# Optimization experiments

Measured on AMD Instinct MI355X. Metric: run time of the kernel, lower is better.

Reference implementation:

```python
import jax, jax.numpy as jnp
import numpy as np

N_NODES = 50000
N_EDGES = 800000
HID = 256
HEADS = 4
HEAD_C = HID // HEADS  # 64
IN_CH = 16
OUT_CH = 4
NEG_SLOPE = 0.2  # PyG GATConv default LeakyReLU slope
LN_EPS = 1e-5


def setup_inputs() -> dict:
    key = jax.random.key(0)
    ks = jax.random.split(key, 12)
    s = 0.05
    return {
        "x": jax.random.normal(ks[0], (N_NODES, IN_CH), dtype=jnp.float32),
        "edge_index": jax.random.randint(ks[1], (2, N_EDGES), 0, N_NODES, dtype=jnp.int64),
        "w_in": jax.random.normal(ks[2], (IN_CH, HID), dtype=jnp.float32) * s,
        "b_in": jnp.zeros((HID,), dtype=jnp.float32),
        "w_gat": jax.random.normal(ks[3], (4, HID, HID), dtype=jnp.float32) * s,
        "att_src": jax.random.normal(ks[4], (4, HEADS, HEAD_C), dtype=jnp.float32) * s,
        "att_dst": jax.random.normal(ks[5], (4, HEADS, HEAD_C), dtype=jnp.float32) * s,
        "b_gat": jnp.zeros((4, HID), dtype=jnp.float32),
        "ln_scale": jnp.ones((4, HID), dtype=jnp.float32),
        "ln_bias": jnp.zeros((4, HID), dtype=jnp.float32),
        "w_out": jax.random.normal(ks[6], (HID, OUT_CH), dtype=jnp.float32) * s,
        "b_out": jnp.zeros((OUT_CH,), dtype=jnp.float32),
    }


def _gat_layer(x, src, dst, W, a_src, a_dst, bias, g, beta):
    """One GATConv(concat, heads=4) + LayerNorm + ELU. x:[N,HID]."""
    n = x.shape[0]
    h = (x @ W).reshape(n, HEADS, HEAD_C)                 # [N,H,C]
    a_s = jnp.einsum("nhc,hc->nh", h, a_src)              # [N,H]
    a_d = jnp.einsum("nhc,hc->nh", h, a_dst)              # [N,H]
    logits = jax.nn.leaky_relu(a_s[src] + a_d[dst], NEG_SLOPE)  # [E,H]
    # segment softmax over destination neighborhoods (self-loops ensure non-empty)
    m = jax.ops.segment_max(logits, dst, num_segments=n)
    e = jnp.exp(logits - m[dst])
    denom = jax.ops.segment_sum(e, dst, num_segments=n)
    alpha = e / (denom[dst] + 1e-16)                      # [E,H]
    msg = alpha[:, :, None] * h[src]                      # [E,H,C]
    out = jax.ops.segment_sum(msg, dst, num_segments=n).reshape(n, HID) + bias
    mu = out.mean(-1, keepdims=True)
    var = out.var(-1, keepdims=True)
    out = (out - mu) * jax.lax.rsqrt(var + LN_EPS) * g + beta
    return jax.nn.elu(out)


def reference(x, edge_index, w_in, b_in, w_gat, att_src, att_dst, b_gat,
              ln_scale, ln_bias, w_out, b_out):
    n = x.shape[0]
    # PyG GATConv adds self-loops by default
    loops = jnp.arange(n, dtype=edge_index.dtype)
    ei = jnp.concatenate([edge_index, jnp.stack([loops, loops])], axis=1)
    src, dst = ei[0], ei[1]

    x = x @ w_in + b_in                                   # input_proj
    h = x
    for l in (0, 1):
        h = _gat_layer(h, src, dst, w_gat[l], att_src[l], att_dst[l],
                       b_gat[l], ln_scale[l], ln_bias[l])
    x = x + h
    h = x
    for l in (2, 3):
        h = _gat_layer(h, src, dst, w_gat[l], att_src[l], att_dst[l],
                       b_gat[l], ln_scale[l], ln_bias[l])
    x = x + h
    return x @ w_out + b_out
```

## Files before the change

kernel.cpp:

```cpp
#include <hip/hip_runtime.h>
#include <math.h>

#define NN 50000
#define E0 800000
#define ET 850000
#define HID 256
#define INCH 16
#define MAXDEG 64

#define NB_P1   416
#define EPB     2048
#define NBUCK   196

#define NB_WT   256
#define NB_IP   6250
#define NB_PREP (NB_P1 + NB_WT + NB_IP)

#define NB_G    782
#define NB_G0   (NBUCK + NB_G)

typedef _Float16 h8 __attribute__((ext_vector_type(8)));
typedef float f32x4 __attribute__((ext_vector_type(4)));

__device__ __forceinline__ void load_lds16(const void* g, void* l) {
    __builtin_amdgcn_global_load_lds(
        (const __attribute__((address_space(1))) unsigned int*)g,
        (__attribute__((address_space(3))) unsigned int*)l, 16, 0, 0);
}

__global__ __launch_bounds__(256) void prep_kernel(
    const float* __restrict__ w_gat, _Float16* __restrict__ WT,
    const float* __restrict__ x, const float* __restrict__ w_in,
    const float* __restrict__ b_in, _Float16* __restrict__ Ph,
    const int* __restrict__ ei, unsigned int* __restrict__ pairs,
    int* __restrict__ cnt_g, int* __restrict__ off_g) {
    __shared__ unsigned int hist[256], pref[256], cur2[256];
    int b = blockIdx.x, t = threadIdx.x;
    if (b < NB_P1) {
        hist[t] = 0;
        __syncthreads();
        unsigned int pk[8];
        int base = b * EPB + t;
#pragma unroll
        for (int k = 0; k < 8; ++k) {
            int e = base + k * 256;
            pk[k] = 0xFFFFFFFFu;
            if (e < ET) {
                int s, d;
                if (e < E0) { s = ei[e]; d = ei[E0 + e]; }
                else        { s = d = e - E0; }
                pk[k] = ((unsigned int)d << 16) | (unsigned int)s;
                atomicAdd(&hist[d >> 8], 1u);
            }
        }
        __syncthreads();
        unsigned int h = hist[t];
        pref[t] = h;
        __syncthreads();
#pragma unroll
        for (int o = 1; o < 256; o <<= 1) {
            unsigned int v = (t >= o) ? pref[t - o] : 0u;
            __syncthreads();
            pref[t] += v;
            __syncthreads();
        }
        unsigned int ex = pref[t] - h;
        cur2[t] = ex;
        if (t < NBUCK) {
            cnt_g[b * NBUCK + t] = (int)h;
            off_g[b * NBUCK + t] = (int)ex;
        }
        __syncthreads();
#pragma unroll
        for (int k = 0; k < 8; ++k) {
            if (pk[k] != 0xFFFFFFFFu) {
                unsigned int g = pk[k] >> 24;
                unsigned int pos = atomicAdd(&cur2[g], 1u);
                pairs[b * EPB + pos] = pk[k];
            }
        }
    } else if (b < NB_P1 + NB_WT) {
        int k = b - NB_P1;
#pragma unroll
        for (int l = 0; l < 4; ++l) {
            float v = w_gat[((size_t)l * 256 + k) * 256 + t];
            WT[((size_t)l * 256 + t) * 256 + k] = (_Float16)v;
        }
    } else {
        int ipb = b - NB_P1 - NB_WT;
        int sub = t >> 5, l32 = t & 31;
        int n = ipb * 8 + sub;
        int c0 = l32 * 8;
        const float* xr = x + n * INCH;
        float a[8];
#pragma unroll
        for (int k = 0; k < 8; k += 4) {
            float4 bb = *(const float4*)(b_in + c0 + k);
            a[k] = bb.x; a[k + 1] = bb.y; a[k + 2] = bb.z; a[k + 3] = bb.w;
        }
#pragma unroll
        for (int k = 0; k < INCH; ++k) {
            float xv = xr[k];
            const float4 w0 = *(const float4*)(w_in + k * 256 + c0);
            const float4 w1 = *(const float4*)(w_in + k * 256 + c0 + 4);
            a[0] += xv * w0.x; a[1] += xv * w0.y; a[2] += xv * w0.z; a[3] += xv * w0.w;
            a[4] += xv * w1.x; a[5] += xv * w1.y; a[6] += xv * w1.z; a[7] += xv * w1.w;
        }
        h8 o;
#pragma unroll
        for (int k = 0; k < 8; ++k) o[k] = (_Float16)a[k];
        *(h8*)(Ph + (size_t)n * 256 + c0) = o;
    }
}

__device__ __forceinline__ void gemm_tile(
    int rb, int cb,
    const _Float16* __restrict__ A, const _Float16* __restrict__ BT,
    _Float16* __restrict__ H, const float* __restrict__ att_s,
    const float* __restrict__ att_d, float* __restrict__ AS, float* __restrict__ AD,
    _Float16* As, _Float16* Bs) {
    int t = threadIdx.x;
    int wv = t >> 6, lane = t & 63;
    int wr = (wv >> 1) * 64, wc = (wv & 1) * 64;
    int lm = lane & 15, lq = lane >> 4;
    f32x4 acc[4][4] = {};

    int rch = lane >> 2;
    int q = lane & 3;

    for (int k0 = 0; k0 < 256; k0 += 32) {
#pragma unroll
        for (int c = 0; c < 2; ++c) {
            int r = wv * 32 + c * 16 + rch;
            int g = q ^ (r & 3);
            int ra = rb + r; if (ra >= NN) ra = NN - 1;
            load_lds16(A + (size_t)ra * 256 + k0 + g * 8,
                       (char*)As + wv * 2048 + c * 1024);
            load_lds16(BT + (size_t)(cb + r) * 256 + k0 + g * 8,
                       (char*)Bs + wv * 2048 + c * 1024);
        }
        __syncthreads();
        h8 af[4], bfr[4];
#pragma unroll
        for (int i = 0; i < 4; ++i) {
            int row = wr + i * 16 + lm;
            af[i] = *(const h8*)((const char*)As + row * 64 + ((lq ^ (row & 3)) * 16));
        }
#pragma unroll
        for (int j = 0; j < 4; ++j) {
            int row = wc + j * 16 + lm;
            bfr[j] = *(const h8*)((const char*)Bs + row * 64 + ((lq ^ (row & 3)) * 16));
        }
#pragma unroll
        for (int i = 0; i < 4; ++i)
#pragma unroll
            for (int j = 0; j < 4; ++j)
                acc[i][j] = __builtin_amdgcn_mfma_f32_16x16x32_f16(af[i], bfr[j], acc[i][j], 0, 0, 0);
        __syncthreads();
    }

    int head = (cb + wc) >> 6;
    float sa[4], sd[4];
#pragma unroll
    for (int j = 0; j < 4; ++j) {
        sa[j] = att_s[head * 64 + j * 16 + lm];
        sd[j] = att_d[head * 64 + j * 16 + lm];
    }
#pragma unroll
    for (int i = 0; i < 4; ++i)
#pragma unroll
        for (int rr = 0; rr < 4; ++rr) {
            float vs = acc[i][0][rr] * sa[0] + acc[i][1][rr] * sa[1]
                     + acc[i][2][rr] * sa[2] + acc[i][3][rr] * sa[3];
            float vd = acc[i][0][rr] * sd[0] + acc[i][1][rr] * sd[1]
                     + acc[i][2][rr] * sd[2] + acc[i][3][rr] * sd[3];
#pragma unroll
            for (int o = 1; o <= 8; o <<= 1) {
                vs += __shfl_xor(vs, o, 64);
                vd += __shfl_xor(vd, o, 64);
            }
            int row = rb + wr + i * 16 + lq * 4 + rr;
            if (lm == 0 && row < NN) {
                AS[row * 4 + head] = vs;
                AD[row * 4 + head] = vd;
            }
        }

#pragma unroll
    for (int i = 0; i < 4; ++i)
#pragma unroll
        for (int j = 0; j < 4; ++j) {
            int col = cb + wc + j * 16 + lm;
#pragma unroll
            for (int rr = 0; rr < 4; ++rr) {
                int row = rb + wr + i * 16 + lq * 4 + rr;
                if (row < NN) H[(size_t)row * 256 + col] = (_Float16)acc[i][j][rr];
            }
        }
}

__global__ __launch_bounds__(256) void gemm_fused_kernel(
    const _Float16* __restrict__ A, const _Float16* __restrict__ BT,
    _Float16* __restrict__ H, const float* __restrict__ att_s,
    const float* __restrict__ att_d, float* __restrict__ AS, float* __restrict__ AD) {
    __shared__ _Float16 As[128 * 32];
    __shared__ _Float16 Bs[128 * 32];
    gemm_tile(blockIdx.x * 128, blockIdx.y * 128, A, BT, H, att_s, att_d, AS, AD, As, Bs);
}

__global__ __launch_bounds__(256) void gemm0_p2_kernel(
    const _Float16* __restrict__ A, const _Float16* __restrict__ BT,
    _Float16* __restrict__ H, const float* __restrict__ att_s,
    const float* __restrict__ att_d, float* __restrict__ AS, float* __restrict__ AD,
    const unsigned int* __restrict__ pairs, const int* __restrict__ cnt_g,
    const int* __restrict__ off_g, int* __restrict__ cursor,
    unsigned short* __restrict__ csr_pad) {
    __shared__ _Float16 As[128 * 32];
    __shared__ _Float16 Bs[128 * 32];
    int b = blockIdx.x;
    if (b < NBUCK) {
        int g = b, t = threadIdx.x;
        unsigned int* curs = (unsigned int*)As;
        curs[t] = 0;
        __syncthreads();
        for (int sb = t; sb < NB_P1; sb += 256) {
            int c = cnt_g[sb * NBUCK + g];
            int o = off_g[sb * NBUCK + g];
            const unsigned int* p = pairs + sb * EPB + o;
            for (int i = 0; i < c; ++i) {
                unsigned int pk = p[i];
                int d = (int)(pk >> 16);
                unsigned int pos = atomicAdd(&curs[d & 255], 1u);
                if (pos < MAXDEG)
                    csr_pad[((size_t)d << 6) + pos] = (unsigned short)(pk & 0xFFFFu);
            }
        }
        __syncthreads();
        int n = (g << 8) + t;
        if (n < NN) cursor[n] = (int)curs[t];
        return;
    }
    int g2 = b - NBUCK;
    gemm_tile((g2 >> 1) * 128, (g2 & 1) * 128, A, BT, H, att_s, att_d, AS, AD, As, Bs);
}

__global__ __launch_bounds__(256) void agg_kernel(
    const _Float16* __restrict__ H, const float4* __restrict__ AS,
    const float4* __restrict__ AD,
    const int* __restrict__ cnt, const unsigned short* __restrict__ csr_pad,
    const float* __restrict__ bias, const float* __restrict__ g, const float* __restrict__ beta,
    const _Float16* __restrict__ res, _Float16* __restrict__ outh,
    const float* __restrict__ wout, const float* __restrict__ bout,
    float* __restrict__ out) {
    int t = threadIdx.x;
    int l32 = t & 31;
    int n = blockIdx.x * 8 + (t >> 5);
    int deg = cnt[n];
    if (deg > MAXDEG) deg = MAXDEG;
    int start = n << 6, end = start + deg;
    float4 adv = AD[n];
    int head = l32 >> 3;
    int c0 = l32 * 8;
    float advh = (head == 0) ? adv.x : (head == 1) ? adv.y : (head == 2) ? adv.z : adv.w;

    float acc[8] = {};
    float acc_e = 0.f;
#pragma unroll 4
    for (int i = start; i < end; ++i) {
        int s = csr_pad[i];
        const float* as = (const float*)&AS[s];
        float v = as[head] + advh;
        v = (v >= 0.f) ? v : 0.2f * v;
        float e = __expf(v);
        acc_e += e;
        h8 hv = *(const h8*)(H + (size_t)s * 256 + c0);
#pragma unroll
        for (int k = 0; k < 8; ++k) acc[k] += e * (float)hv[k];
    }
    float dinv = 1.f / (acc_e + 1e-16f);

    float val[8];
#pragma unroll
    for (int k = 0; k < 8; k += 4) {
        float4 bb = *(const float4*)(bias + c0 + k);
        val[k]     = acc[k]     * dinv + bb.x;
        val[k + 1] = acc[k + 1] * dinv + bb.y;
        val[k + 2] = acc[k + 2] * dinv + bb.z;
        val[k + 3] = acc[k + 3] * dinv + bb.w;
    }

    float s1 = 0.f, s2 = 0.f;
#pragma unroll
    for (int k = 0; k < 8; ++k) { s1 += val[k]; s2 += val[k] * val[k]; }
#pragma unroll
    for (int o = 16; o >= 1; o >>= 1) {
        s1 += __shfl_xor(s1, o, 64);
        s2 += __shfl_xor(s2, o, 64);
    }
    float mu = s1 * (1.f / 256.f);
    float var = s2 * (1.f / 256.f) - mu * mu;
    float rs = rsqrtf(var + 1e-5f);

    float y[8];
#pragma unroll
    for (int k = 0; k < 8; k += 4) {
        float4 g4 = *(const float4*)(g + c0 + k);
        float4 b4 = *(const float4*)(beta + c0 + k);
        y[k]     = (val[k]     - mu) * rs * g4.x + b4.x;
        y[k + 1] = (val[k + 1] - mu) * rs * g4.y + b4.y;
        y[k + 2] = (val[k + 2] - mu) * rs * g4.z + b4.z;
        y[k + 3] = (val[k + 3] - mu) * rs * g4.w + b4.w;
    }
#pragma unroll
    for (int k = 0; k < 8; ++k) y[k] = (y[k] > 0.f) ? y[k] : (__expf(y[k]) - 1.f);
    if (res) {
        h8 r0 = *(const h8*)(res + (size_t)n * 256 + c0);
#pragma unroll
        for (int k = 0; k < 8; ++k) y[k] += (float)r0[k];
    }
    if (wout) {
        float o0 = 0.f, o1 = 0.f, o2 = 0.f, o3 = 0.f;
#pragma unroll
        for (int k = 0; k < 8; ++k) {
            float4 wv = *(const float4*)(wout + (size_t)(c0 + k) * 4);
            o0 += y[k] * wv.x; o1 += y[k] * wv.y; o2 += y[k] * wv.z; o3 += y[k] * wv.w;
        }
#pragma unroll
        for (int o = 16; o >= 1; o >>= 1) {
            o0 += __shfl_xor(o0, o, 64);
            o1 += __shfl_xor(o1, o, 64);
            o2 += __shfl_xor(o2, o, 64);
            o3 += __shfl_xor(o3, o, 64);
        }
        if (l32 == 0) {
            float4 ov = make_float4(o0 + bout[0], o1 + bout[1], o2 + bout[2], o3 + bout[3]);
            *(float4*)(out + (size_t)n * 4) = ov;
        }
    } else {
        h8 o0;
#pragma unroll
        for (int k = 0; k < 8; ++k) o0[k] = (_Float16)y[k];
        *(h8*)(outh + (size_t)n * 256 + c0) = o0;
    }
}

extern "C" void kernel_launch(void* const* d_in, const int* in_sizes, int n_in,
                              void* d_out, int out_size, void* d_ws, size_t ws_size,
                              hipStream_t stream) {
    const float* x       = (const float*)d_in[0];
    const int*   ei      = (const int*)  d_in[1];
    const float* w_in    = (const float*)d_in[2];
    const float* b_in    = (const float*)d_in[3];
    const float* w_gat   = (const float*)d_in[4];
    const float* att_src = (const float*)d_in[5];
    const float* att_dst = (const float*)d_in[6];
    const float* b_gat   = (const float*)d_in[7];
    const float* ln_g    = (const float*)d_in[8];
    const float* ln_b    = (const float*)d_in[9];
    const float* w_out   = (const float*)d_in[10];
    const float* b_out   = (const float*)d_in[11];
    float* out = (float*)d_out;

    char* ws = (char*)d_ws;
    size_t off = 0;
    auto alloc = [&](size_t bytes) {
        void* p = ws + off;
        off += (bytes + 255) & ~(size_t)255;
        return p;
    };
    _Float16*       Ph      = (_Float16*)alloc((size_t)NN * HID * 2);
    _Float16*       Ch      = (_Float16*)alloc((size_t)NN * HID * 2);
    _Float16*       Gh      = (_Float16*)alloc((size_t)NN * HID * 2);
    _Float16*       H       = (_Float16*)alloc((size_t)NN * HID * 2);
    _Float16*       WT      = (_Float16*)alloc((size_t)4 * HID * HID * 2);
    float*          ASAD    = (float*)alloc((size_t)NN * 8 * 4);
    int*            cursor  = (int*)alloc((size_t)NN * 4);
    unsigned short* csr_pad = (unsigned short*)alloc((size_t)NN * MAXDEG * 2);
    unsigned int*   pairs   = (unsigned int*)alloc((size_t)NB_P1 * EPB * 4);
    int*            cnt_g   = (int*)alloc((size_t)NB_P1 * NBUCK * 4);
    int*            off_g   = (int*)alloc((size_t)NB_P1 * NBUCK * 4);

    float* AS = ASAD;
    float* AD = ASAD + (size_t)NN * 4;

    const dim3 GEMM_GRID(391, 2);
    const int NB_AGG = NN / 8;

    prep_kernel<<<NB_PREP, 256, 0, stream>>>(w_gat, WT, x, w_in, b_in, Ph,
                                             ei, pairs, cnt_g, off_g);

    gemm0_p2_kernel<<<NB_G0, 256, 0, stream>>>(
        Ph, WT, H, att_src, att_dst, AS, AD, pairs, cnt_g, off_g, cursor, csr_pad);
    agg_kernel<<<NB_AGG, 256, 0, stream>>>(
        H, (const float4*)AS, (const float4*)AD, cursor, csr_pad,
        b_gat, ln_g, ln_b, nullptr, Gh, nullptr, nullptr, nullptr);

    auto run_layer = [&](const _Float16* inh, int l, const _Float16* res, _Float16* outh,
                         const float* wo, const float* bo) {
        gemm_fused_kernel<<<GEMM_GRID, 256, 0, stream>>>(
            inh, WT + (size_t)l * HID * HID, H,
            att_src + l * 256, att_dst + l * 256, AS, AD);
        agg_kernel<<<NB_AGG, 256, 0, stream>>>(
            H, (const float4*)AS, (const float4*)AD, cursor, csr_pad,
            b_gat + l * 256, ln_g + l * 256, ln_b + l * 256, res, outh, wo, bo,
            wo ? out : nullptr);
    };

    run_layer(Gh, 1, Ph,      Ch, nullptr, nullptr);
    run_layer(Ch, 2, nullptr, Gh, nullptr, nullptr);
    run_layer(Gh, 3, Ch,      Ph, w_out,   b_out);
}
```

Baseline: 527.7 us.

## Assign one wavefront per node and precompute edge weights in LDS

The aggregation kernel now uses a full 64-lane wavefront per destination node instead of half a wave. Each lane loads 4 channels instead of 8. Before the gather loop, the lanes compute the neighbor indices and all four heads' exp(leaky_relu) logits in parallel and store them in LDS. This takes the per-edge AS load and exp off the serial gather loop and doubles the parallelism per node. In exchange it uses narrower 8-byte H loads, twice as many blocks, an extra reduction step, and some LDS usage. There is no barrier between the LDS writes and reads, which is safe only because each wave reads only its own region.

```diff
diff --git a/kernel.cpp b/kernel.cpp
--- a/kernel.cpp
+++ b/kernel.cpp
@@ -20,6 +20,7 @@
 #define NB_G0   (NBUCK + NB_G)
 
 typedef _Float16 h8 __attribute__((ext_vector_type(8)));
+typedef _Float16 h4 __attribute__((ext_vector_type(4)));
 typedef float f32x4 __attribute__((ext_vector_type(4)));
 
 __device__ __forceinline__ void load_lds16(const void* g, void* l) {
@@ -252,48 +253,58 @@
     const _Float16* __restrict__ res, _Float16* __restrict__ outh,
     const float* __restrict__ wout, const float* __restrict__ bout,
     float* __restrict__ out) {
+    __shared__ float eLs[4][256];
+    __shared__ int   sLs[4][64];
     int t = threadIdx.x;
-    int l32 = t & 31;
-    int n = blockIdx.x * 8 + (t >> 5);
+    int wv = t >> 6, lane = t & 63;
+    int n = blockIdx.x * 4 + wv;
+    int head = lane >> 4;
+    int c0 = lane * 4;
+    float* eL = eLs[wv];
+    int*   sL = sLs[wv];
+
     int deg = cnt[n];
     if (deg > MAXDEG) deg = MAXDEG;
-    int start = n << 6, end = start + deg;
     float4 adv = AD[n];
-    int head = l32 >> 3;
-    int c0 = l32 * 8;
-    float advh = (head == 0) ? adv.x : (head == 1) ? adv.y : (head == 2) ? adv.z : adv.w;
-
-    float acc[8] = {};
-    float acc_e = 0.f;
+
+    float4 e4 = make_float4(0.f, 0.f, 0.f, 0.f);
+    int sv = 0;
+    if (lane < deg) {
+        sv = csr_pad[(n << 6) + lane];
+        float4 as = AS[sv];
+        float v0 = as.x + adv.x; v0 = (v0 >= 0.f) ? v0 : 0.2f * v0;
+        float v1 = as.y + adv.y; v1 = (v1 >= 0.f) ? v1 : 0.2f * v1;
+        float v2 = as.z + adv.z; v2 = (v2 >= 0.f) ? v2 : 0.2f * v2;
+        float v3 = as.w + adv.w; v3 = (v3 >= 0.f) ? v3 : 0.2f * v3;
+        e4 = make_float4(__expf(v0), __expf(v1), __expf(v2), __expf(v3));
+    }
+    sL[lane] = sv;
+    *(float4*)(eL + c0) = e4;
+
+    float acc0 = 0.f, acc1 = 0.f, acc2 = 0.f, acc3 = 0.f, acc_e = 0.f;
 #pragma unroll 4
-    for (int i = start; i < end; ++i) {
-        int s = csr_pad[i];
-        const float* as = (const float*)&AS[s];
-        float v = as[head] + advh;
-        v = (v >= 0.f) ? v : 0.2f * v;
-        float e = __expf(v);
+    for (int i = 0; i < deg; ++i) {
+        float e = eL[i * 4 + head];
+        int s = sL[i];
+        h4 hv = *(const h4*)(H + (size_t)s * 256 + c0);
         acc_e += e;
-        h8 hv = *(const h8*)(H + (size_t)s * 256 + c0);
-#pragma unroll
-        for (int k = 0; k < 8; ++k) acc[k] += e * (float)hv[k];
+        acc0 += e * (float)hv[0];
+        acc1 += e * (float)hv[1];
+        acc2 += e * (float)hv[2];
+        acc3 += e * (float)hv[3];
     }
     float dinv = 1.f / (acc_e + 1e-16f);
 
-    float val[8];
-#pragma unroll
-    for (int k = 0; k < 8; k += 4) {
-        float4 bb = *(const float4*)(bias + c0 + k);
-        val[k]     = acc[k]     * dinv + bb.x;
-        val[k + 1] = acc[k + 1] * dinv + bb.y;
-        val[k + 2] = acc[k + 2] * dinv + bb.z;
-        val[k + 3] = acc[k + 3] * dinv + bb.w;
-    }
-
-    float s1 = 0.f, s2 = 0.f;
-#pragma unroll
-    for (int k = 0; k < 8; ++k) { s1 += val[k]; s2 += val[k] * val[k]; }
-#pragma unroll
-    for (int o = 16; o >= 1; o >>= 1) {
+    float4 bb = *(const float4*)(bias + c0);
+    float val0 = acc0 * dinv + bb.x;
+    float val1 = acc1 * dinv + bb.y;
+    float val2 = acc2 * dinv + bb.z;
+    float val3 = acc3 * dinv + bb.w;
+
+    float s1 = val0 + val1 + val2 + val3;
+    float s2 = val0 * val0 + val1 * val1 + val2 * val2 + val3 * val3;
+#pragma unroll
+    for (int o = 32; o >= 1; o >>= 1) {
         s1 += __shfl_xor(s1, o, 64);
         s2 += __shfl_xor(s2, o, 64);
     }
@@ -301,46 +312,45 @@
     float var = s2 * (1.f / 256.f) - mu * mu;
     float rs = rsqrtf(var + 1e-5f);
 
-    float y[8];
-#pragma unroll
-    for (int k = 0; k < 8; k += 4) {
-        float4 g4 = *(const float4*)(g + c0 + k);
-        float4 b4 = *(const float4*)(beta + c0 + k);
-        y[k]     = (val[k]     - mu) * rs * g4.x + b4.x;
-        y[k + 1] = (val[k + 1] - mu) * rs * g4.y + b4.y;
-        y[k + 2] = (val[k + 2] - mu) * rs * g4.z + b4.z;
-        y[k + 3] = (val[k + 3] - mu) * rs * g4.w + b4.w;
-    }
-#pragma unroll
-    for (int k = 0; k < 8; ++k) y[k] = (y[k] > 0.f) ? y[k] : (__expf(y[k]) - 1.f);
+    float4 g4 = *(const float4*)(g + c0);
+    float4 b4 = *(const float4*)(beta + c0);
+    float y0 = (val0 - mu) * rs * g4.x + b4.x;
+    float y1 = (val1 - mu) * rs * g4.y + b4.y;
+    float y2 = (val2 - mu) * rs * g4.z + b4.z;
+    float y3 = (val3 - mu) * rs * g4.w + b4.w;
+    y0 = (y0 > 0.f) ? y0 : (__expf(y0) - 1.f);
+    y1 = (y1 > 0.f) ? y1 : (__expf(y1) - 1.f);
+    y2 = (y2 > 0.f) ? y2 : (__expf(y2) - 1.f);
+    y3 = (y3 > 0.f) ? y3 : (__expf(y3) - 1.f);
     if (res) {
-        h8 r0 = *(const h8*)(res + (size_t)n * 256 + c0);
-#pragma unroll
-        for (int k = 0; k < 8; ++k) y[k] += (float)r0[k];
+        h4 r0 = *(const h4*)(res + (size_t)n * 256 + c0);
+        y0 += (float)r0[0]; y1 += (float)r0[1]; y2 += (float)r0[2]; y3 += (float)r0[3];
     }
     if (wout) {
-        float o0 = 0.f, o1 = 0.f, o2 = 0.f, o3 = 0.f;
-#pragma unroll
-        for (int k = 0; k < 8; ++k) {
-            float4 wv = *(const float4*)(wout + (size_t)(c0 + k) * 4);
-            o0 += y[k] * wv.x; o1 += y[k] * wv.y; o2 += y[k] * wv.z; o3 += y[k] * wv.w;
-        }
-#pragma unroll
-        for (int o = 16; o >= 1; o >>= 1) {
+        float4 w0 = *(const float4*)(wout + (size_t)(c0 + 0) * 4);
+        float4 w1 = *(const float4*)(wout + (size_t)(c0 + 1) * 4);
+        float4 w2 = *(const float4*)(wout + (size_t)(c0 + 2) * 4);
+        float4 w3 = *(const float4*)(wout + (size_t)(c0 + 3) * 4);
+        float o0 = y0 * w0.x + y1 * w1.x + y2 * w2.x + y3 * w3.x;
+        float o1 = y0 * w0.y + y1 * w1.y + y2 * w2.y + y3 * w3.y;
+        float o2 = y0 * w0.z + y1 * w1.z + y2 * w2.z + y3 * w3.z;
+        float o3 = y0 * w0.w + y1 * w1.w + y2 * w2.w + y3 * w3.w;
+#pragma unroll
+        for (int o = 32; o >= 1; o >>= 1) {
             o0 += __shfl_xor(o0, o, 64);
             o1 += __shfl_xor(o1, o, 64);
             o2 += __shfl_xor(o2, o, 64);
             o3 += __shfl_xor(o3, o, 64);
         }
-        if (l32 == 0) {
+        if (lane == 0) {
             float4 ov = make_float4(o0 + bout[0], o1 + bout[1], o2 + bout[2], o3 + bout[3]);
             *(float4*)(out + (size_t)n * 4) = ov;
         }
     } else {
-        h8 o0;
-#pragma unroll
-        for (int k = 0; k < 8; ++k) o0[k] = (_Float16)y[k];
-        *(h8*)(outh + (size_t)n * 256 + c0) = o0;
+        h4 o0;
+        o0[0] = (_Float16)y0; o0[1] = (_Float16)y1;
+        o0[2] = (_Float16)y2; o0[3] = (_Float16)y3;
+        *(h4*)(outh + (size_t)n * 256 + c0) = o0;
     }
 }
 
@@ -384,7 +394,7 @@
     float* AD = ASAD + (size_t)NN * 4;
 
     const dim3 GEMM_GRID(391, 2);
-    const int NB_AGG = NN / 8;
+    const int NB_AGG = NN / 4;
 
     prep_kernel<<<NB_PREP, 256, 0, stream>>>(w_gat, WT, x, w_in, b_in, Ph,
                                              ei, pairs, cnt_g, off_g);
```

Result: faster. 511.1 us (-3.1%).

## Double-buffer GEMM LDS, remap tiles, and precompute edge weights per wave in aggregation

Applied to the files above, without the earlier changes.

The GEMM tile loop now double-buffers its LDS staging, issuing the next K-slice's global-to-LDS loads before the current slice's MFMAs so load latency can overlap compute. Both GEMM kernels switch to a 1D grid with a block-to-tile mapping that groups the two column halves of neighbouring row blocks together, aiming for better reuse of A rows in cache. The aggregation kernel now gives each node a full 64-lane wave: every lane computes the exp attention weight for one edge once for all four heads and stores it in LDS, then the two half-waves process alternating edges and are combined with a shuffle. This removes the per-head recomputation of the exponentials and the serial index loads, at the cost of extra LDS use, twice as many aggregation blocks, and idle half-waves during the epilogue.

```diff
diff --git a/kernel.cpp b/kernel.cpp
--- a/kernel.cpp
+++ b/kernel.cpp
@@ -16,10 +16,11 @@
 #define NB_IP   6250
 #define NB_PREP (NB_P1 + NB_WT + NB_IP)
 
-#define NB_G    782
+#define NB_G    784
 #define NB_G0   (NBUCK + NB_G)
 
 typedef _Float16 h8 __attribute__((ext_vector_type(8)));
+typedef _Float16 h4 __attribute__((ext_vector_type(4)));
 typedef float f32x4 __attribute__((ext_vector_type(4)));
 
 __device__ __forceinline__ void load_lds16(const void* g, void* l) {
@@ -128,28 +129,34 @@
     int rch = lane >> 2;
     int q = lane & 3;
 
-    for (int k0 = 0; k0 < 256; k0 += 32) {
+    auto stage = [&](int k0, int buf) {
 #pragma unroll
         for (int c = 0; c < 2; ++c) {
             int r = wv * 32 + c * 16 + rch;
             int g = q ^ (r & 3);
             int ra = rb + r; if (ra >= NN) ra = NN - 1;
             load_lds16(A + (size_t)ra * 256 + k0 + g * 8,
-                       (char*)As + wv * 2048 + c * 1024);
+                       (char*)As + buf * 8192 + wv * 2048 + c * 1024);
             load_lds16(BT + (size_t)(cb + r) * 256 + k0 + g * 8,
-                       (char*)Bs + wv * 2048 + c * 1024);
-        }
-        __syncthreads();
+                       (char*)Bs + buf * 8192 + wv * 2048 + c * 1024);
+        }
+    };
+
+    stage(0, 0);
+    __syncthreads();
+    int cur = 0;
+    for (int k0 = 0; k0 < 256; k0 += 32) {
+        if (k0 + 32 < 256) stage(k0 + 32, cur ^ 1);
         h8 af[4], bfr[4];
 #pragma unroll
         for (int i = 0; i < 4; ++i) {
             int row = wr + i * 16 + lm;
-            af[i] = *(const h8*)((const char*)As + row * 64 + ((lq ^ (row & 3)) * 16));
+            af[i] = *(const h8*)((const char*)As + cur * 8192 + row * 64 + ((lq ^ (row & 3)) * 16));
         }
 #pragma unroll
         for (int j = 0; j < 4; ++j) {
             int row = wc + j * 16 + lm;
-            bfr[j] = *(const h8*)((const char*)Bs + row * 64 + ((lq ^ (row & 3)) * 16));
+            bfr[j] = *(const h8*)((const char*)Bs + cur * 8192 + row * 64 + ((lq ^ (row & 3)) * 16));
         }
 #pragma unroll
         for (int i = 0; i < 4; ++i)
@@ -157,6 +164,7 @@
             for (int j = 0; j < 4; ++j)
                 acc[i][j] = __builtin_amdgcn_mfma_f32_16x16x32_f16(af[i], bfr[j], acc[i][j], 0, 0, 0);
         __syncthreads();
+        cur ^= 1;
     }
 
     int head = (cb + wc) >> 6;
@@ -199,13 +207,23 @@
         }
 }
 
+__device__ __forceinline__ bool gemm_map(int b, int& rb, int& cb) {
+    int r = (b >> 4) * 8 + (b & 7);
+    int h = (b >> 3) & 1;
+    if (r >= 391) return false;
+    rb = r * 128; cb = h * 128;
+    return true;
+}
+
 __global__ __launch_bounds__(256) void gemm_fused_kernel(
     const _Float16* __restrict__ A, const _Float16* __restrict__ BT,
     _Float16* __restrict__ H, const float* __restrict__ att_s,
     const float* __restrict__ att_d, float* __restrict__ AS, float* __restrict__ AD) {
-    __shared__ _Float16 As[128 * 32];
-    __shared__ _Float16 Bs[128 * 32];
-    gemm_tile(blockIdx.x * 128, blockIdx.y * 128, A, BT, H, att_s, att_d, AS, AD, As, Bs);
+    __shared__ _Float16 As[2 * 128 * 32];
+    __shared__ _Float16 Bs[2 * 128 * 32];
+    int rb, cb;
+    if (!gemm_map(blockIdx.x, rb, cb)) return;
+    gemm_tile(rb, cb, A, BT, H, att_s, att_d, AS, AD, As, Bs);
 }
 
 __global__ __launch_bounds__(256) void gemm0_p2_kernel(
@@ -215,8 +233,8 @@
     const unsigned int* __restrict__ pairs, const int* __restrict__ cnt_g,
     const int* __restrict__ off_g, int* __restrict__ cursor,
     unsigned short* __restrict__ csr_pad) {
-    __shared__ _Float16 As[128 * 32];
-    __shared__ _Float16 Bs[128 * 32];
+    __shared__ _Float16 As[2 * 128 * 32];
+    __shared__ _Float16 Bs[2 * 128 * 32];
     int b = blockIdx.x;
     if (b < NBUCK) {
         int g = b, t = threadIdx.x;
@@ -240,8 +258,9 @@
         if (n < NN) cursor[n] = (int)curs[t];
         return;
     }
-    int g2 = b - NBUCK;
-    gemm_tile((g2 >> 1) * 128, (g2 & 1) * 128, A, BT, H, att_s, att_d, AS, AD, As, Bs);
+    int rb, cb;
+    if (!gemm_map(b - NBUCK, rb, cb)) return;
+    gemm_tile(rb, cb, A, BT, H, att_s, att_d, AS, AD, As, Bs);
 }
 
 __global__ __launch_bounds__(256) void agg_kernel(
@@ -252,31 +271,50 @@
     const _Float16* __restrict__ res, _Float16* __restrict__ outh,
     const float* __restrict__ wout, const float* __restrict__ bout,
     float* __restrict__ out) {
+    __shared__ float eLs[4][256];
+    __shared__ int   sLs[4][64];
     int t = threadIdx.x;
-    int l32 = t & 31;
-    int n = blockIdx.x * 8 + (t >> 5);
+    int wv = t >> 6, lane = t & 63;
+    int n = blockIdx.x * 4 + wv;
+    float* eL = eLs[wv];
+    int*   sL = sLs[wv];
+
     int deg = cnt[n];
     if (deg > MAXDEG) deg = MAXDEG;
-    int start = n << 6, end = start + deg;
     float4 adv = AD[n];
-    int head = l32 >> 3;
-    int c0 = l32 * 8;
-    float advh = (head == 0) ? adv.x : (head == 1) ? adv.y : (head == 2) ? adv.z : adv.w;
-
+
+    float4 e4 = make_float4(0.f, 0.f, 0.f, 0.f);
+    int sv = 0;
+    if (lane < deg) {
+        sv = csr_pad[(n << 6) + lane];
+        float4 as = AS[sv];
+        float v0 = as.x + adv.x; v0 = (v0 >= 0.f) ? v0 : 0.2f * v0;
+        float v1 = as.y + adv.y; v1 = (v1 >= 0.f) ? v1 : 0.2f * v1;
+        float v2 = as.z + adv.z; v2 = (v2 >= 0.f) ? v2 : 0.2f * v2;
+        float v3 = as.w + adv.w; v3 = (v3 >= 0.f) ? v3 : 0.2f * v3;
+        e4 = make_float4(__expf(v0), __expf(v1), __expf(v2), __expf(v3));
+    }
+    sL[lane] = sv;
+    *(float4*)(eL + lane * 4) = e4;
+
+    int half = lane >> 5;
+    int l5 = lane & 31;
+    int head = l5 >> 3;
+    int c0 = l5 * 8;
     float acc[8] = {};
     float acc_e = 0.f;
-#pragma unroll 4
-    for (int i = start; i < end; ++i) {
-        int s = csr_pad[i];
-        const float* as = (const float*)&AS[s];
-        float v = as[head] + advh;
-        v = (v >= 0.f) ? v : 0.2f * v;
-        float e = __expf(v);
+#pragma unroll 2
+    for (int i = half; i < deg; i += 2) {
+        float e = eL[i * 4 + head];
+        int s = sL[i];
+        h8 hv = *(const h8*)(H + (size_t)s * 256 + c0);
         acc_e += e;
-        h8 hv = *(const h8*)(H + (size_t)s * 256 + c0);
 #pragma unroll
         for (int k = 0; k < 8; ++k) acc[k] += e * (float)hv[k];
     }
+#pragma unroll
+    for (int k = 0; k < 8; ++k) acc[k] += __shfl_xor(acc[k], 32, 64);
+    acc_e += __shfl_xor(acc_e, 32, 64);
     float dinv = 1.f / (acc_e + 1e-16f);
 
     float val[8];
@@ -322,8 +360,8 @@
         float o0 = 0.f, o1 = 0.f, o2 = 0.f, o3 = 0.f;
 #pragma unroll
         for (int k = 0; k < 8; ++k) {
-            float4 wv = *(const float4*)(wout + (size_t)(c0 + k) * 4);
-            o0 += y[k] * wv.x; o1 += y[k] * wv.y; o2 += y[k] * wv.z; o3 += y[k] * wv.w;
+            float4 wv4 = *(const float4*)(wout + (size_t)(c0 + k) * 4);
+            o0 += y[k] * wv4.x; o1 += y[k] * wv4.y; o2 += y[k] * wv4.z; o3 += y[k] * wv4.w;
         }
 #pragma unroll
         for (int o = 16; o >= 1; o >>= 1) {
@@ -332,15 +370,17 @@
             o2 += __shfl_xor(o2, o, 64);
             o3 += __shfl_xor(o3, o, 64);
         }
-        if (l32 == 0) {
+        if (lane == 0) {
             float4 ov = make_float4(o0 + bout[0], o1 + bout[1], o2 + bout[2], o3 + bout[3]);
             *(float4*)(out + (size_t)n * 4) = ov;
         }
     } else {
-        h8 o0;
-#pragma unroll
-        for (int k = 0; k < 8; ++k) o0[k] = (_Float16)y[k];
-        *(h8*)(outh + (size_t)n * 256 + c0) = o0;
+        if (half == 0) {
+            h8 o0;
+#pragma unroll
+            for (int k = 0; k < 8; ++k) o0[k] = (_Float16)y[k];
+            *(h8*)(outh + (size_t)n * 256 + c0) = o0;
+        }
     }
 }
 
@@ -383,8 +423,7 @@
     float* AS = ASAD;
     float* AD = ASAD + (size_t)NN * 4;
 
-    const dim3 GEMM_GRID(391, 2);
-    const int NB_AGG = NN / 8;
+    const int NB_AGG = NN / 4;
 
     prep_kernel<<<NB_PREP, 256, 0, stream>>>(w_gat, WT, x, w_in, b_in, Ph,
                                              ei, pairs, cnt_g, off_g);
@@ -397,7 +436,7 @@
 
     auto run_layer = [&](const _Float16* inh, int l, const _Float16* res, _Float16* outh,
                          const float* wo, const float* bo) {
-        gemm_fused_kernel<<<GEMM_GRID, 256, 0, stream>>>(
+        gemm_fused_kernel<<<NB_G, 256, 0, stream>>>(
             inh, WT + (size_t)l * HID * HID, H,
             att_src + l * 256, att_dst + l * 256, AS, AD);
         agg_kernel<<<NB_AGG, 256, 0, stream>>>(
```

New measurement: 519.7 us. No clear change (-1.5%).
